# Kernel tuning notes

Measured on AMD Instinct MI355X. Metric: run time of the kernel, lower is better.

Reference implementation:

```python
import jax, jax.numpy as jnp
import numpy as np

HID = 768
NSPLITS = 12
HEAD_RATIO = 2
H = NSPLITS // HEAD_RATIO          # 6 attention heads
D = HID // NSPLITS                 # 64 head size
AH = H * D                         # 384 all_head_size
KS = 9                             # conv kernel size
PAD = (KS - 1) // 2
B, S = 4, 1024


def setup_inputs() -> dict:
    key = jax.random.key(0)
    ks = jax.random.split(key, 16)
    std = 0.02
    inp = {
        "Q": jax.random.normal(ks[0], (B, S, HID), jnp.float32),
        "K": jax.random.normal(ks[1], (B, S, HID), jnp.float32),
        "V": jax.random.normal(ks[2], (B, S, HID), jnp.float32),
        "td": jax.random.uniform(ks[3], (B, S), jnp.float32),
        "mask": jax.random.randint(ks[4], (B, S), 0, 2, jnp.int32),
        # projection weights, applied as x @ W (in, out)
        "Wq": jax.random.normal(ks[5], (HID, AH), jnp.float32) * std,
        "Wk": jax.random.normal(ks[6], (HID, AH), jnp.float32) * std,
        "Wv": jax.random.normal(ks[7], (HID, AH), jnp.float32) * std,
        # separable conv: depthwise (HID, KS), pointwise (AH, HID), bias (AH,)
        "dw_w": jax.random.normal(ks[8], (HID, KS), jnp.float32) * std,
        "pw_w": jax.random.normal(ks[9], (AH, HID), jnp.float32) * std,
        "sep_b": jnp.zeros((AH,), jnp.float32),
        # conv_kernel_layer Linear(AH -> H*KS)
        "ck_W": jax.random.normal(ks[10], (AH, H * KS), jnp.float32) * std,
        "ck_b": jnp.zeros((H * KS,), jnp.float32),
        # conv_out_layer Linear(HID -> AH)
        "co_W": jax.random.normal(ks[11], (HID, AH), jnp.float32) * std,
        "co_b": jnp.zeros((AH,), jnp.float32),
        # gammas init to zeros as in torch module
        "gammas": jnp.zeros((H, 1, 1), jnp.float32),
    }
    return inp


def dist_func(scores, td, am, gammas):
    # scores: [B,H,S,S]; am: [B,1,1,S] bool key mask; entirely non-differentiable.
    s = scores.shape[-1]
    dt = scores.dtype
    amf = am.astype(dt)
    p = jax.nn.softmax(jnp.where(am, scores, -1e8), axis=-1) * amf
    distcum = jnp.cumsum(p, axis=-1)
    disttotal = jnp.sum(p, axis=-1, keepdims=True)
    # |j - i| position distance
    pos = jnp.abs(jnp.arange(s)[None, :] - jnp.arange(s)[:, None]).astype(dt)
    dist_scores = jnp.sqrt(jnp.clip((disttotal - distcum) * pos[None, None], 0.0, None))
    gamma = -jax.nn.softplus(gammas)[None]  # (1,H,1,1)
    total_effect = jnp.clip(jnp.exp(dist_scores * gamma), 1e-5, 1e5)
    # time-distance effect on strictly-lower-triangular positions
    tdn = td / jnp.maximum(jnp.linalg.norm(td, axis=-1, keepdims=True), 1e-12)
    td_scores = jnp.broadcast_to(tdn[:, None, None, :], scores.shape)
    td_sm = jax.nn.softmax(jnp.where(am, td_scores, -1e4), axis=-1)
    lower = jnp.tril(jnp.ones((s, s), dt), -1)  # (triu == 0)
    return jax.lax.stop_gradient(total_effect - td_sm * lower[None, None])


def reference(Q, K, V, td, mask, Wq, Wk, Wv, dw_w, pw_w, sep_b, ck_W, ck_b, co_W, co_b, gammas):
    b, s, hid = Q.shape
    mq = Q @ Wq  # (B,S,AH)
    mk = K @ Wk
    mv = V @ Wv
    # SeparableConv1D over sequence dim of K
    x = jnp.transpose(K, (0, 2, 1))  # (B,HID,S)
    dw = jax.lax.conv_general_dilated(
        x, dw_w[:, None, :], window_strides=(1,), padding=[(PAD, PAD)],
        feature_group_count=hid, dimension_numbers=("NCH", "OIH", "NCH"))
    pw = jnp.einsum("bcs,oc->bos", dw, pw_w) + sep_b[None, :, None]
    mkc = jnp.transpose(pw, (0, 2, 1))  # (B,S,AH)

    q = mq.reshape(b, s, H, D).transpose(0, 2, 1, 3)
    k = mk.reshape(b, s, H, D).transpose(0, 2, 1, 3)
    v = mv.reshape(b, s, H, D).transpose(0, 2, 1, 3)

    # dynamic span convolution
    conv_attn = mkc * mq                                   # (B,S,AH)
    ck = (conv_attn @ ck_W + ck_b).reshape(b, s, H, KS)
    ck = jax.nn.softmax(ck, axis=-1)                       # per-position kernel
    co = V @ co_W + co_b                                   # (B,S,AH)
    co_pad = jnp.pad(co, ((0, 0), (PAD, PAD), (0, 0)))
    idx = jnp.arange(s)[:, None] + jnp.arange(KS)[None, :]  # (S,KS)
    unf = co_pad[:, idx, :].reshape(b, s, KS, H, D)         # sliding window gather
    conv_out = jnp.einsum("bskhd,bshk->bshd", unf, ck)      # (B,S,H,D)

    # attention with distance decay
    scores = jnp.einsum("bhid,bhjd->bhij", q, k) / np.float32(np.sqrt(D))
    am = (mask[:, None, None, :] != 0)  # (B,1,1,S) key mask
    total_effect = dist_func(scores, td, am, gammas)
    scores = jnp.where(am, scores * total_effect, -1e8)
    probs = jax.nn.softmax(scores, axis=-1)
    ctx = jnp.einsum("bhij,bhjd->bhid", probs, v).transpose(0, 2, 1, 3)  # (B,S,H,D)

    out = jnp.concatenate([ctx, conv_out], axis=2).reshape(b, s, HEAD_RATIO * AH)
    return out
```

## Files before the change

kernel.cpp:

```cpp
#include <hip/hip_runtime.h>
#include <hip/hip_bf16.h>

#define HIDC 768
#define Hh   6
#define Dd   64
#define AHc  384
#define KSc  9
#define PADc 4
#define Bb   4
#define Ss   1024
#define MRr  (Bb * Ss)

typedef __attribute__((ext_vector_type(8))) __bf16 bf16x8;
typedef __attribute__((ext_vector_type(4))) __bf16 bf16x4;
typedef __attribute__((ext_vector_type(4))) float  f32x4;

__device__ __forceinline__ void gl_lds16(const void* g, void* l) {
    __builtin_amdgcn_global_load_lds(
        (const __attribute__((address_space(1))) void*)g,
        (__attribute__((address_space(3))) void*)l, 16, 0, 0);
}

__device__ __forceinline__ void split8(const float* p, bf16x8& hi, bf16x8& lo) {
    float4 x0 = *(const float4*)p;
    float4 x1 = *(const float4*)(p + 4);
    float xs[8] = {x0.x, x0.y, x0.z, x0.w, x1.x, x1.y, x1.z, x1.w};
#pragma unroll
    for (int e = 0; e < 8; ++e) {
        __bf16 hv = (__bf16)xs[e];
        hi[e] = hv;
        lo[e] = (__bf16)(xs[e] - (float)hv);
    }
}

__device__ __forceinline__ void split8r(const float* xs, bf16x8& hi, bf16x8& lo) {
#pragma unroll
    for (int e = 0; e < 8; ++e) {
        __bf16 hv = (__bf16)xs[e];
        hi[e] = hv;
        lo[e] = (__bf16)(xs[e] - (float)hv);
    }
}

__device__ __forceinline__ bf16x8 cvt8(const float* p) {
    float4 x0 = *(const float4*)p;
    float4 x1 = *(const float4*)(p + 4);
    float xs[8] = {x0.x, x0.y, x0.z, x0.w, x1.x, x1.y, x1.z, x1.w};
    bf16x8 h;
#pragma unroll
    for (int e = 0; e < 8; ++e) h[e] = (__bf16)xs[e];
    return h;
}

__global__ void k_depthwise(const float* __restrict__ Kin, const float* __restrict__ dww,
                            __bf16* __restrict__ dwbf) {
    int idx = blockIdx.x * 256 + threadIdx.x;
    if (idx >= Bb * Ss * HIDC / 4) return;
    int c4 = idx % (HIDC / 4);
    int s  = (idx / (HIDC / 4)) % Ss;
    int b  = idx / ((HIDC / 4) * Ss);
    int c  = c4 * 4;
    float wv[4][KSc];
#pragma unroll
    for (int j = 0; j < 4; ++j)
#pragma unroll
        for (int k = 0; k < KSc; ++k) wv[j][k] = dww[(c + j) * KSc + k];
    float4 acc = {0.f, 0.f, 0.f, 0.f};
#pragma unroll
    for (int k = 0; k < KSc; ++k) {
        int sp = s + k - PADc;
        if (sp >= 0 && sp < Ss) {
            float4 v = *(const float4*)&Kin[(size_t)(b * Ss + sp) * HIDC + c];
            acc.x += v.x * wv[0][k]; acc.y += v.y * wv[1][k];
            acc.z += v.z * wv[2][k]; acc.w += v.w * wv[3][k];
        }
    }
    bf16x4 o = {(__bf16)acc.x, (__bf16)acc.y, (__bf16)acc.z, (__bf16)acc.w};
    *(bf16x4*)(dwbf + (size_t)idx * 4) = o;
}

__global__ __launch_bounds__(256) void k_wsplit_t(const float* __restrict__ Wq, const float* __restrict__ Wk,
                                                  const float* __restrict__ Wv, const float* __restrict__ coW,
                                                  __bf16* __restrict__ Whi, __bf16* __restrict__ Wlo) {
    int z = blockIdx.z;
    const float* src = (z == 0) ? Wq : (z == 1) ? Wk : (z == 2) ? Wv : coW;
    int n0 = blockIdx.x * 64, k0 = blockIdx.y * 64;
    int tid = threadIdx.x;
    int r = tid >> 2, cq = tid & 3;
    __shared__ float tile[64][65];
#pragma unroll
    for (int e = 0; e < 4; ++e) {
        float4 v = *(const float4*)&src[(size_t)(k0 + r) * AHc + n0 + cq * 16 + e * 4];
        tile[r][cq * 16 + e * 4 + 0] = v.x;
        tile[r][cq * 16 + e * 4 + 1] = v.y;
        tile[r][cq * 16 + e * 4 + 2] = v.z;
        tile[r][cq * 16 + e * 4 + 3] = v.w;
    }
    __syncthreads();
    float x[16];
#pragma unroll
    for (int e = 0; e < 16; ++e) x[e] = tile[cq * 16 + e][r];
    bf16x8 h0, l0, h1, l1;
    split8r(x, h0, l0);
    split8r(x + 8, h1, l1);
    size_t dst = ((size_t)(z * AHc + n0 + r)) * HIDC + k0 + cq * 16;
    *(bf16x8*)(Whi + dst)     = h0;
    *(bf16x8*)(Whi + dst + 8) = h1;
    *(bf16x8*)(Wlo + dst)     = l0;
    *(bf16x8*)(Wlo + dst + 8) = l1;
}

__global__ void k_wsplit_c(const float* __restrict__ pww,
                           __bf16* __restrict__ Whi, __bf16* __restrict__ Wlo) {
    int idx = blockIdx.x * 256 + threadIdx.x;
    if (idx >= AHc * HIDC / 8) return;
    bf16x8 hi, lo;
    split8(pww + (size_t)idx * 8, hi, lo);
    size_t dst = (size_t)4 * AHc * HIDC + (size_t)idx * 8;
    *(bf16x8*)(Whi + dst) = hi;
    *(bf16x8*)(Wlo + dst) = lo;
}

__global__ void k_absplit(const float* __restrict__ Q, const float* __restrict__ V,
                          __bf16* __restrict__ qbf, __bf16* __restrict__ vbf) {
    const int n8 = MRr * HIDC / 8;
    int idx = blockIdx.x * 256 + threadIdx.x;
    if (idx >= 2 * n8) return;
    if (idx < n8) {
        *(bf16x8*)(qbf + (size_t)idx * 8) = cvt8(Q + (size_t)idx * 8);
    } else {
        int i = idx - n8;
        *(bf16x8*)(vbf + (size_t)i * 8) = cvt8(V + (size_t)i * 8);
    }
}

__global__ void k_qkvsplit(const float* __restrict__ mq, __bf16* __restrict__ qh) {
    int idx = blockIdx.x * 256 + threadIdx.x;
    if (idx >= MRr * AHc / 8) return;
    *(bf16x8*)(qh + (size_t)idx * 8) = cvt8(mq + (size_t)idx * 8);
}

__global__ __launch_bounds__(256) void k_vtrans(const float* __restrict__ mv,
                                                __bf16* __restrict__ vt) {
    int s0 = blockIdx.x * 64;
    int h = blockIdx.y % Hh, b = blockIdx.y / Hh;
    int tid = threadIdx.x;
    int r = tid >> 2, cq = tid & 3;
    __shared__ float tile[64][65];
    const float* src = mv + (size_t)(b * Ss + s0 + r) * AHc + h * Dd + cq * 16;
#pragma unroll
    for (int e = 0; e < 4; ++e) {
        float4 v = *(const float4*)(src + e * 4);
        tile[r][cq * 16 + e * 4 + 0] = v.x;
        tile[r][cq * 16 + e * 4 + 1] = v.y;
        tile[r][cq * 16 + e * 4 + 2] = v.z;
        tile[r][cq * 16 + e * 4 + 3] = v.w;
    }
    __syncthreads();
    bf16x8 o0, o1;
#pragma unroll
    for (int e = 0; e < 8; ++e) {
        o0[e] = (__bf16)tile[cq * 16 + e][r];
        o1[e] = (__bf16)tile[cq * 16 + 8 + e][r];
    }
    __bf16* dst = vt + ((size_t)((b * Hh + h) * Dd + r)) * Ss + s0 + cq * 16;
    *(bf16x8*)dst       = o0;
    *(bf16x8*)(dst + 8) = o1;
}

__global__ void k_bias(const float* __restrict__ cob, const float* __restrict__ sepb,
                       float* __restrict__ biasb) {
    int idx = blockIdx.x * 256 + threadIdx.x;
    if (idx >= 5 * AHc) return;
    int z = idx / AHc, n = idx % AHc;
    biasb[idx] = (z == 3) ? cob[n] : (z == 4) ? sepb[n] : 0.f;
}

__global__ __launch_bounds__(256) void k_gemm5(
        const __bf16* __restrict__ qbf, const float* __restrict__ Kin,
        const __bf16* __restrict__ vbf, const __bf16* __restrict__ dwbf,
        const __bf16* __restrict__ Whi, const __bf16* __restrict__ Wlo,
        const float* __restrict__ biasb, float* __restrict__ Call,
        __bf16* __restrict__ kh, __bf16* __restrict__ kl) {
    __shared__ __attribute__((aligned(16))) __bf16 As [128 * 32];
    __shared__ __attribute__((aligned(16))) __bf16 BsH[128 * 32];
    __shared__ __attribute__((aligned(16))) __bf16 BsL[128 * 32];

    int wg = blockIdx.x + 3 * (blockIdx.y + 32 * blockIdx.z);
    int n2 = (wg & 7) * 60 + (wg >> 3);
    int bxx = n2 % 3, byy = (n2 / 3) % 32, z = n2 / 96;

    int m0 = byy * 128, n0 = bxx * 128;
    int tid = threadIdx.x;
    int wave = tid >> 6, lane = tid & 63, quad = lane >> 4, l15 = lane & 15;

    int lrow = lane >> 2;
    int lswz = 8 * ((lane & 3) ^ (lrow & 3));

    int brow = wave * 32 + lrow;
    const __bf16* BhG0 = Whi + ((size_t)(z * AHc + n0 + brow)) * HIDC + lswz;
    const __bf16* BhG1 = BhG0 + (size_t)16 * HIDC;
    const __bf16* BlG0 = Wlo + ((size_t)(z * AHc + n0 + brow)) * HIDC + lswz;
    const __bf16* BlG1 = BlG0 + (size_t)16 * HIDC;
    __bf16* BhL0 = BsH + (wave * 2 + 0) * 512;
    __bf16* BhL1 = BsH + (wave * 2 + 1) * 512;
    __bf16* BlL0 = BsL + (wave * 2 + 0) * 512;
    __bf16* BlL1 = BsL + (wave * 2 + 1) * 512;

    const __bf16* Abf = (z == 0) ? qbf : (z == 4) ? dwbf : vbf;
    const __bf16* AG0 = Abf + ((size_t)(m0 + wave * 32 + lrow)) * HIDC + lswz;
    const __bf16* AG1 = AG0 + (size_t)16 * HIDC;
    __bf16* AL0 = As + (wave * 2 + 0) * 512;
    __bf16* AL1 = As + (wave * 2 + 1) * 512;

    int sr = tid >> 1;
    int sk = (tid & 1) * 16;
    const float* Arow = Kin + (size_t)(m0 + sr) * HIDC + sk;
    int g0 = sk >> 3;
    int d0 = sr * 32 + ((g0       ^ (sr & 3)) * 8);
    int d1 = sr * 32 + (((g0 + 1) ^ (sr & 3)) * 8);

    int swz = (quad ^ (l15 & 3)) * 8;
    f32x4 acc[4][4] = {};

    for (int k0 = 0; k0 < HIDC; k0 += 32) {
        if (z == 1) {
            const float* ap = Arow + k0;
            *(bf16x8*)&As[d0] = cvt8(ap);
            *(bf16x8*)&As[d1] = cvt8(ap + 8);
        } else {
            gl_lds16(AG0 + k0, AL0);
            gl_lds16(AG1 + k0, AL1);
        }
        gl_lds16(BhG0 + k0, BhL0);
        gl_lds16(BhG1 + k0, BhL1);
        gl_lds16(BlG0 + k0, BlL0);
        gl_lds16(BlG1 + k0, BlL1);
        __syncthreads();

        int mrow = (wave >> 1) * 64 + l15;
        int nrow = (wave & 1) * 64 + l15;
        bf16x8 ah[4], bh[4], bl[4];
#pragma unroll
        for (int mt = 0; mt < 4; ++mt)
            ah[mt] = *(bf16x8*)&As[(mrow + mt * 16) * 32 + swz];
#pragma unroll
        for (int nt = 0; nt < 4; ++nt) {
            bh[nt] = *(bf16x8*)&BsH[(nrow + nt * 16) * 32 + swz];
            bl[nt] = *(bf16x8*)&BsL[(nrow + nt * 16) * 32 + swz];
        }
#pragma unroll
        for (int mt = 0; mt < 4; ++mt)
#pragma unroll
            for (int nt = 0; nt < 4; ++nt) {
                acc[mt][nt] = __builtin_amdgcn_mfma_f32_16x16x32_bf16(ah[mt], bh[nt], acc[mt][nt], 0, 0, 0);
                acc[mt][nt] = __builtin_amdgcn_mfma_f32_16x16x32_bf16(ah[mt], bl[nt], acc[mt][nt], 0, 0, 0);
            }
        __syncthreads();
    }

    if (z == 1) {
#pragma unroll
        for (int nt = 0; nt < 4; ++nt) {
            int n = n0 + (wave & 1) * 64 + nt * 16 + l15;
#pragma unroll
            for (int mt = 0; mt < 4; ++mt) {
#pragma unroll
                for (int r = 0; r < 4; ++r) {
                    int m = m0 + (wave >> 1) * 64 + mt * 16 + quad * 4 + r;
                    float v = acc[mt][nt][r];
                    __bf16 hv = (__bf16)v;
                    kh[(size_t)m * AHc + n] = hv;
                    kl[(size_t)m * AHc + n] = (__bf16)(v - (float)hv);
                }
            }
        }
    } else {
        float* Cz = Call + (size_t)z * MRr * AHc;
        const float* bz = biasb + z * AHc;
#pragma unroll
        for (int nt = 0; nt < 4; ++nt) {
            int n = n0 + (wave & 1) * 64 + nt * 16 + l15;
            float bias = bz[n];
#pragma unroll
            for (int mt = 0; mt < 4; ++mt) {
#pragma unroll
                for (int r = 0; r < 4; ++r) {
                    int m = m0 + (wave >> 1) * 64 + mt * 16 + quad * 4 + r;
                    Cz[(size_t)m * AHc + n] = acc[mt][nt][r] + bias;
                }
            }
        }
    }
}

__global__ __launch_bounds__(64) void k_ck(const float* __restrict__ mkc, const float* __restrict__ mq,
                                           const float* __restrict__ ckW, const float* __restrict__ ckb,
                                           float* __restrict__ ck_sm) {
    int row = blockIdx.x;
    int tid = threadIdx.x;
    __shared__ float ca[AHc];
    __shared__ float ckv[Hh * KSc];
    for (int o = tid; o < AHc; o += 64)
        ca[o] = mkc[row * AHc + o] * mq[row * AHc + o];
    __syncthreads();
    if (tid < Hh * KSc) {
        float acc = ckb[tid];
        for (int o = 0; o < AHc; ++o)
            acc += ca[o] * ckW[o * (Hh * KSc) + tid];
        ckv[tid] = acc;
    }
    __syncthreads();
    if (tid < Hh) {
        float m = -3e38f;
#pragma unroll
        for (int k = 0; k < KSc; ++k) m = fmaxf(m, ckv[tid * KSc + k]);
        float e[KSc];
        float s = 0.f;
#pragma unroll
        for (int k = 0; k < KSc; ++k) { e[k] = expf(ckv[tid * KSc + k] - m); s += e[k]; }
        float inv = 1.f / s;
#pragma unroll
        for (int k = 0; k < KSc; ++k) ck_sm[(row * Hh + tid) * KSc + k] = e[k] * inv;
    }
}

__global__ void k_convout(const float* __restrict__ co, const float* __restrict__ ck_sm,
                          float* __restrict__ out) {
    int idx = blockIdx.x * 256 + threadIdx.x;
    if (idx >= Bb * Ss * AHc / 4) return;
    int d4 = idx & 15;
    int h  = (idx >> 4) % Hh;
    int s  = (idx / (AHc / 4)) % Ss;
    int b  = idx / ((AHc / 4) * Ss);
    int row = b * Ss + s;
    const float* ck = ck_sm + (size_t)(row * Hh + h) * KSc;
    float4 acc = {0.f, 0.f, 0.f, 0.f};
#pragma unroll
    for (int k = 0; k < KSc; ++k) {
        int sp = s + k - PADc;
        if (sp >= 0 && sp < Ss) {
            float4 v = *(const float4*)&co[(size_t)(b * Ss + sp) * AHc + h * Dd + d4 * 4];
            float wv = ck[k];
            acc.x += wv * v.x; acc.y += wv * v.y; acc.z += wv * v.z; acc.w += wv * v.w;
        }
    }
    *(float4*)&out[(size_t)row * (2 * AHc) + AHc + h * Dd + d4 * 4] = acc;
}

__global__ __launch_bounds__(256) void k_td(const float* __restrict__ td, const int* __restrict__ mask,
                                            float* __restrict__ td_sm) {
    int b = blockIdx.x;
    int tid = threadIdx.x;
    __shared__ float red[256];
    __shared__ float tv[Ss];
    float ls = 0.f;
    for (int j = tid; j < Ss; j += 256) {
        float v = td[b * Ss + j];
        tv[j] = v;
        ls += v * v;
    }
    red[tid] = ls; __syncthreads();
    for (int s = 128; s > 0; s >>= 1) { if (tid < s) red[tid] += red[tid + s]; __syncthreads(); }
    float norm = fmaxf(sqrtf(red[0]), 1e-12f);
    __syncthreads();
    float lm = -3e38f;
    for (int j = tid; j < Ss; j += 256) {
        float v = mask[b * Ss + j] ? tv[j] / norm : -1e4f;
        tv[j] = v;
        lm = fmaxf(lm, v);
    }
    red[tid] = lm; __syncthreads();
    for (int s = 128; s > 0; s >>= 1) { if (tid < s) red[tid] = fmaxf(red[tid], red[tid + s]); __syncthreads(); }
    float m = red[0]; __syncthreads();
    float lsum = 0.f;
    for (int j = tid; j < Ss; j += 256) {
        float e = expf(tv[j] - m);
        tv[j] = e;
        lsum += e;
    }
    red[tid] = lsum; __syncthreads();
    for (int s = 128; s > 0; s >>= 1) { if (tid < s) red[tid] += red[tid + s]; __syncthreads(); }
    float inv = 1.f / red[0];
    __syncthreads();
    for (int j = tid; j < Ss; j += 256)
        td_sm[b * Ss + j] = tv[j] * inv;
}

__device__ __forceinline__ int scix(int m, int j) {
    return m * 1024 + (j ^ (((m ^ (j >> 6)) & 7) << 2));
}

__global__ __launch_bounds__(512) void k_attn(const __bf16* __restrict__ qh,
                                              const __bf16* __restrict__ kh, const __bf16* __restrict__ kl,
                                              const __bf16* __restrict__ vt,
                                              const int* __restrict__ mask,
                                              const float* __restrict__ td_sm, const float* __restrict__ gammas,
                                              float* __restrict__ out) {
    __shared__ float sc[16 * 1024];
    int wg = blockIdx.x + 64 * blockIdx.y;
    int n  = (wg & 7) * 192 + (wg >> 3);
    int bx = n & 63, by = n >> 6;
    int i0 = bx * 16;
    int h = by % Hh, b = by / Hh;
    int tid = threadIdx.x;
    int w = tid >> 6, lane = tid & 63, quad = lane >> 4, l15 = lane & 15;
    int jw = w * 128;

    bf16x8 a_hi[2];
    {
        size_t qoff = (size_t)(b * Ss + i0 + l15) * AHc + h * Dd + quad * 8;
        a_hi[0] = *(const bf16x8*)(qh + qoff);
        a_hi[1] = *(const bf16x8*)(qh + qoff + 32);
    }
#pragma unroll 2
    for (int t = 0; t < 8; ++t) {
        int jt = jw + t * 16;
        size_t koff = (size_t)(b * Ss + jt + l15) * AHc + h * Dd + quad * 8;
        f32x4 acc = {0.f, 0.f, 0.f, 0.f};
#pragma unroll
        for (int kc = 0; kc < 2; ++kc) {
            bf16x8 khv = *(const bf16x8*)(kh + koff + kc * 32);
            bf16x8 klv = *(const bf16x8*)(kl + koff + kc * 32);
            acc = __builtin_amdgcn_mfma_f32_16x16x32_bf16(a_hi[kc], khv, acc, 0, 0, 0);
            acc = __builtin_amdgcn_mfma_f32_16x16x32_bf16(a_hi[kc], klv, acc, 0, 0, 0);
        }
#pragma unroll
        for (int r = 0; r < 4; ++r)
            sc[scix(quad * 4 + r, jt + l15)] = acc[r] * 0.125f;
    }
    __syncthreads();

    const int* mrow = mask + b * Ss;
    const float* tdrow = td_sm + b * Ss;
    float gamma = -log1pf(expf(gammas[h]));
    int jb = lane << 4;
    __attribute__((aligned(16))) int marr[16];
    {
        const int4* mp = (const int4*)(mrow + jb);
#pragma unroll
        for (int k = 0; k < 4; ++k) ((int4*)marr)[k] = mp[k];
    }
    __attribute__((aligned(16))) float tdv[16];
    {
        const float4* tp = (const float4*)(tdrow + jb);
#pragma unroll
        for (int k = 0; k < 4; ++k) ((float4*)tdv)[k] = tp[k];
    }

#pragma unroll
    for (int r4 = 0; r4 < 2; ++r4) {
        int m = w * 2 + r4;
        int i = i0 + m;
        __attribute__((aligned(16))) float s[16];
        float p[16];
#pragma unroll
        for (int g = 0; g < 4; ++g)
            *(f32x4*)(s + 4 * g) = *(const f32x4*)&sc[scix(m, jb + 4 * g)];
        float mx = -1e30f;
#pragma unroll
        for (int jj = 0; jj < 16; ++jj) mx = fmaxf(mx, marr[jj] ? s[jj] : -1e30f);
        mx = fmaxf(mx, __shfl_xor(mx, 1));  mx = fmaxf(mx, __shfl_xor(mx, 2));
        mx = fmaxf(mx, __shfl_xor(mx, 4));  mx = fmaxf(mx, __shfl_xor(mx, 8));
        mx = fmaxf(mx, __shfl_xor(mx, 16)); mx = fmaxf(mx, __shfl_xor(mx, 32));
#pragma unroll
        for (int jj = 0; jj < 16; ++jj) p[jj] = marr[jj] ? __expf(s[jj] - mx) : 0.f;
#pragma unroll
        for (int jj = 1; jj < 16; ++jj) p[jj] += p[jj - 1];
        float t = p[15];
        float incl = t;
#pragma unroll
        for (int dlt = 1; dlt < 64; dlt <<= 1) {
            float v = __shfl_up(incl, dlt);
            if (lane >= dlt) incl += v;
        }
        float off = incl - t;
        float tot = __shfl(incl, 63);
        float inv = 1.f / fmaxf(tot, 1e-30f);
        float mx2 = -1e30f;
#pragma unroll
        for (int jj = 0; jj < 16; ++jj) {
            int j = jb + jj;
            float cum = p[jj] + off;
            float pos = fabsf((float)(j - i));
            float ds = sqrtf(fmaxf((tot - cum) * inv * pos, 0.f));
            float te = fminf(fmaxf(__expf(ds * gamma), 1e-5f), 1e5f);
            float mult = te - ((j < i) ? tdv[jj] : 0.f);
            float s2 = marr[jj] ? s[jj] * mult : -1e8f;
            s[jj] = s2;
            mx2 = fmaxf(mx2, s2);
        }
        mx2 = fmaxf(mx2, __shfl_xor(mx2, 1));  mx2 = fmaxf(mx2, __shfl_xor(mx2, 2));
        mx2 = fmaxf(mx2, __shfl_xor(mx2, 4));  mx2 = fmaxf(mx2, __shfl_xor(mx2, 8));
        mx2 = fmaxf(mx2, __shfl_xor(mx2, 16)); mx2 = fmaxf(mx2, __shfl_xor(mx2, 32));
        float sm = 0.f;
#pragma unroll
        for (int jj = 0; jj < 16; ++jj) { s[jj] = __expf(s[jj] - mx2); sm += s[jj]; }
        sm += __shfl_xor(sm, 1);  sm += __shfl_xor(sm, 2);
        sm += __shfl_xor(sm, 4);  sm += __shfl_xor(sm, 8);
        sm += __shfl_xor(sm, 16); sm += __shfl_xor(sm, 32);
        float inv2 = 1.f / sm;
#pragma unroll
        for (int jj = 0; jj < 16; ++jj) s[jj] *= inv2;
#pragma unroll
        for (int g = 0; g < 4; ++g)
            *(f32x4*)&sc[scix(m, jb + 4 * g)] = *(const f32x4*)(s + 4 * g);
    }
    __syncthreads();

    f32x4 oacc[4] = {};
    const __bf16* vtb = vt + (size_t)(b * Hh + h) * Dd * Ss;
#pragma unroll
    for (int kc = 0; kc < 4; ++kc) {
        int j0 = jw + kc * 32 + quad * 8;
        __attribute__((aligned(16))) float x[8];
        *(f32x4*)x       = *(const f32x4*)&sc[scix(l15, j0)];
        *(f32x4*)(x + 4) = *(const f32x4*)&sc[scix(l15, j0 + 4)];
        bf16x8 p_hi, p_lo;
        split8r(x, p_hi, p_lo);
#pragma unroll
        for (int nt = 0; nt < 4; ++nt) {
            int d = nt * 16 + l15;
            bf16x8 vv = *(const bf16x8*)(vtb + (size_t)d * Ss + j0);
            oacc[nt] = __builtin_amdgcn_mfma_f32_16x16x32_bf16(p_hi, vv, oacc[nt], 0, 0, 0);
            oacc[nt] = __builtin_amdgcn_mfma_f32_16x16x32_bf16(p_lo, vv, oacc[nt], 0, 0, 0);
        }
    }
    __syncthreads();
#pragma unroll
    for (int nt = 0; nt < 4; ++nt)
#pragma unroll
        for (int r = 0; r < 4; ++r)
            sc[w * 1024 + (quad * 4 + r) * 64 + nt * 16 + l15] = oacc[nt][r];
    __syncthreads();
#pragma unroll
    for (int e = 0; e < 2; ++e) {
        int idx = e * 512 + tid;
        int m = idx >> 6, dd = idx & 63;
        float v = 0.f;
#pragma unroll
        for (int ww = 0; ww < 8; ++ww) v += sc[ww * 1024 + idx];
        out[(size_t)(b * Ss + i0 + m) * (2 * AHc) + h * Dd + dd] = v;
    }
}

extern "C" void kernel_launch(void* const* d_in, const int* in_sizes, int n_in,
                              void* d_out, int out_size, void* d_ws, size_t ws_size,
                              hipStream_t stream) {
    const float* Q    = (const float*)d_in[0];
    const float* Kin  = (const float*)d_in[1];
    const float* V    = (const float*)d_in[2];
    const float* td   = (const float*)d_in[3];
    const int*   mask = (const int*)d_in[4];
    const float* Wq   = (const float*)d_in[5];
    const float* Wk   = (const float*)d_in[6];
    const float* Wv   = (const float*)d_in[7];
    const float* dww  = (const float*)d_in[8];
    const float* pww  = (const float*)d_in[9];
    const float* sepb = (const float*)d_in[10];
    const float* ckW  = (const float*)d_in[11];
    const float* ckb  = (const float*)d_in[12];
    const float* coW  = (const float*)d_in[13];
    const float* cob  = (const float*)d_in[14];
    const float* gam  = (const float*)d_in[15];
    float* out = (float*)d_out;
    float* ws = (float*)d_ws;

    float* mq    = ws;
    float* mks   = mq    + (size_t)MRr * AHc;
    float* mv    = mks   + (size_t)MRr * AHc;
    float* co    = mv    + (size_t)MRr * AHc;
    float* mkc   = co    + (size_t)MRr * AHc;
    float* dwr   = mkc   + (size_t)MRr * AHc;
    float* cksm  = dwr   + (size_t)MRr * HIDC;
    float* tdsm  = cksm  + (size_t)MRr * Hh * KSc;
    float* biasb = tdsm  + (size_t)Bb * Ss;

    __bf16* dwbf = (__bf16*)dwr;
    __bf16* qbf  = (__bf16*)(dwr + (size_t)MRr * HIDC / 2);
    __bf16* qh   = (__bf16*)dwr;
    __bf16* vt   = (__bf16*)(dwr + (size_t)MRr * HIDC / 2);
    __bf16* kh = (__bf16*)mks;
    __bf16* kl = kh + (size_t)MRr * AHc;

    __bf16* Whi = (__bf16*)d_out;
    __bf16* Wlo = Whi + (size_t)5 * AHc * HIDC;
    __bf16* vbf = Wlo + (size_t)5 * AHc * HIDC;

    dim3 gt(AHc / 64, HIDC / 64, 4);
    k_wsplit_t<<<gt, 256, 0, stream>>>(Wq, Wk, Wv, coW, Whi, Wlo);
    k_wsplit_c<<<(AHc * HIDC / 8 + 255) / 256, 256, 0, stream>>>(pww, Whi, Wlo);
    k_absplit<<<(2 * MRr * HIDC / 8 + 255) / 256, 256, 0, stream>>>(Q, V, qbf, vbf);
    k_depthwise<<<(MRr * HIDC / 4 + 255) / 256, 256, 0, stream>>>(Kin, dww, dwbf);
    k_bias<<<(5 * AHc + 255) / 256, 256, 0, stream>>>(cob, sepb, biasb);

    dim3 gg(AHc / 128, MRr / 128, 5);
    k_gemm5<<<gg, 256, 0, stream>>>(qbf, Kin, vbf, dwbf, Whi, Wlo, biasb, mq, kh, kl);

    k_qkvsplit<<<(MRr * AHc / 8 + 255) / 256, 256, 0, stream>>>(mq, qh);
    k_vtrans<<<dim3(Ss / 64, Bb * Hh), 256, 0, stream>>>(mv, vt);
    k_ck<<<MRr, 64, 0, stream>>>(mkc, mq, ckW, ckb, cksm);
    k_convout<<<(MRr * AHc / 4 + 255) / 256, 256, 0, stream>>>(co, cksm, out);
    k_td<<<Bb, 256, 0, stream>>>(td, mask, tdsm);

    dim3 ga(Ss / 16, Bb * Hh);
    k_attn<<<ga, 512, 0, stream>>>(qh, kh, kl, vt, mask, tdsm, gam, out);
}
```

Baseline: 303.4 us.

## Fold small prep kernels together and emit bf16 Q/V-transposed from GEMM epilogue

Merges the depthwise conv with the Q/V bf16 casts into one launch, and merges the pointwise-weight split, bias setup and td softmax into one misc kernel. The GEMM epilogue now writes bf16 Q directly (alongside fp32 mq needed by the conv path) and writes V already transposed as bf16. This removes the separate qkvsplit and vtrans kernels and their fp32 re-reads. Workspace layout changes so vt/qh live in the former mv region. The scattered transposed stores of V from the epilogue may be less coalesced than the tiled transpose.

Result: faster. 281.7 us (-7.2%).

```diff
diff --git a/kernel.cpp b/kernel.cpp
--- a/kernel.cpp
+++ b/kernel.cpp
@@ -52,31 +52,44 @@
     return h;
 }
 
-__global__ void k_depthwise(const float* __restrict__ Kin, const float* __restrict__ dww,
-                            __bf16* __restrict__ dwbf) {
-    int idx = blockIdx.x * 256 + threadIdx.x;
-    if (idx >= Bb * Ss * HIDC / 4) return;
-    int c4 = idx % (HIDC / 4);
-    int s  = (idx / (HIDC / 4)) % Ss;
-    int b  = idx / ((HIDC / 4) * Ss);
-    int c  = c4 * 4;
-    float wv[4][KSc];
-#pragma unroll
-    for (int j = 0; j < 4; ++j)
-#pragma unroll
-        for (int k = 0; k < KSc; ++k) wv[j][k] = dww[(c + j) * KSc + k];
-    float4 acc = {0.f, 0.f, 0.f, 0.f};
-#pragma unroll
-    for (int k = 0; k < KSc; ++k) {
-        int sp = s + k - PADc;
-        if (sp >= 0 && sp < Ss) {
-            float4 v = *(const float4*)&Kin[(size_t)(b * Ss + sp) * HIDC + c];
-            acc.x += v.x * wv[0][k]; acc.y += v.y * wv[1][k];
-            acc.z += v.z * wv[2][k]; acc.w += v.w * wv[3][k];
-        }
-    }
-    bf16x4 o = {(__bf16)acc.x, (__bf16)acc.y, (__bf16)acc.z, (__bf16)acc.w};
-    *(bf16x4*)(dwbf + (size_t)idx * 4) = o;
+__global__ void k_dwab(const float* __restrict__ Kin, const float* __restrict__ dww,
+                       const float* __restrict__ Q, const float* __restrict__ V,
+                       __bf16* __restrict__ dwbf,
+                       __bf16* __restrict__ qbf, __bf16* __restrict__ vbf) {
+    int bid = blockIdx.x;
+    if (bid < 3072) {
+        int idx = bid * 256 + threadIdx.x;
+        int c4 = idx % (HIDC / 4);
+        int s  = (idx / (HIDC / 4)) % Ss;
+        int b  = idx / ((HIDC / 4) * Ss);
+        int c  = c4 * 4;
+        float wv[4][KSc];
+#pragma unroll
+        for (int j = 0; j < 4; ++j)
+#pragma unroll
+            for (int k = 0; k < KSc; ++k) wv[j][k] = dww[(c + j) * KSc + k];
+        float4 acc = {0.f, 0.f, 0.f, 0.f};
+#pragma unroll
+        for (int k = 0; k < KSc; ++k) {
+            int sp = s + k - PADc;
+            if (sp >= 0 && sp < Ss) {
+                float4 v = *(const float4*)&Kin[(size_t)(b * Ss + sp) * HIDC + c];
+                acc.x += v.x * wv[0][k]; acc.y += v.y * wv[1][k];
+                acc.z += v.z * wv[2][k]; acc.w += v.w * wv[3][k];
+            }
+        }
+        bf16x4 o = {(__bf16)acc.x, (__bf16)acc.y, (__bf16)acc.z, (__bf16)acc.w};
+        *(bf16x4*)(dwbf + (size_t)idx * 4) = o;
+    } else {
+        const int n8 = MRr * HIDC / 8;
+        int idx = (bid - 3072) * 256 + threadIdx.x;
+        if (idx < n8) {
+            *(bf16x8*)(qbf + (size_t)idx * 8) = cvt8(Q + (size_t)idx * 8);
+        } else {
+            int i = idx - n8;
+            *(bf16x8*)(vbf + (size_t)i * 8) = cvt8(V + (size_t)i * 8);
+        }
+    }
 }
 
 __global__ __launch_bounds__(256) void k_wsplit_t(const float* __restrict__ Wq, const float* __restrict__ Wk,
@@ -110,70 +123,64 @@
     *(bf16x8*)(Wlo + dst + 8) = l1;
 }
 
-__global__ void k_wsplit_c(const float* __restrict__ pww,
-                           __bf16* __restrict__ Whi, __bf16* __restrict__ Wlo) {
-    int idx = blockIdx.x * 256 + threadIdx.x;
-    if (idx >= AHc * HIDC / 8) return;
-    bf16x8 hi, lo;
-    split8(pww + (size_t)idx * 8, hi, lo);
-    size_t dst = (size_t)4 * AHc * HIDC + (size_t)idx * 8;
-    *(bf16x8*)(Whi + dst) = hi;
-    *(bf16x8*)(Wlo + dst) = lo;
-}
-
-__global__ void k_absplit(const float* __restrict__ Q, const float* __restrict__ V,
-                          __bf16* __restrict__ qbf, __bf16* __restrict__ vbf) {
-    const int n8 = MRr * HIDC / 8;
-    int idx = blockIdx.x * 256 + threadIdx.x;
-    if (idx >= 2 * n8) return;
-    if (idx < n8) {
-        *(bf16x8*)(qbf + (size_t)idx * 8) = cvt8(Q + (size_t)idx * 8);
-    } else {
-        int i = idx - n8;
-        *(bf16x8*)(vbf + (size_t)i * 8) = cvt8(V + (size_t)i * 8);
-    }
-}
-
-__global__ void k_qkvsplit(const float* __restrict__ mq, __bf16* __restrict__ qh) {
-    int idx = blockIdx.x * 256 + threadIdx.x;
-    if (idx >= MRr * AHc / 8) return;
-    *(bf16x8*)(qh + (size_t)idx * 8) = cvt8(mq + (size_t)idx * 8);
-}
-
-__global__ __launch_bounds__(256) void k_vtrans(const float* __restrict__ mv,
-                                                __bf16* __restrict__ vt) {
-    int s0 = blockIdx.x * 64;
-    int h = blockIdx.y % Hh, b = blockIdx.y / Hh;
+__global__ __launch_bounds__(256) void k_misc(const float* __restrict__ pww,
+                                              const float* __restrict__ cob, const float* __restrict__ sepb,
+                                              const float* __restrict__ td, const int* __restrict__ mask,
+                                              __bf16* __restrict__ Whi, __bf16* __restrict__ Wlo,
+                                              float* __restrict__ biasb, float* __restrict__ td_sm) {
+    int bid = blockIdx.x;
     int tid = threadIdx.x;
-    int r = tid >> 2, cq = tid & 3;
-    __shared__ float tile[64][65];
-    const float* src = mv + (size_t)(b * Ss + s0 + r) * AHc + h * Dd + cq * 16;
-#pragma unroll
-    for (int e = 0; e < 4; ++e) {
-        float4 v = *(const float4*)(src + e * 4);
-        tile[r][cq * 16 + e * 4 + 0] = v.x;
-        tile[r][cq * 16 + e * 4 + 1] = v.y;
-        tile[r][cq * 16 + e * 4 + 2] = v.z;
-        tile[r][cq * 16 + e * 4 + 3] = v.w;
-    }
-    __syncthreads();
-    bf16x8 o0, o1;
-#pragma unroll
-    for (int e = 0; e < 8; ++e) {
-        o0[e] = (__bf16)tile[cq * 16 + e][r];
-        o1[e] = (__bf16)tile[cq * 16 + 8 + e][r];
-    }
-    __bf16* dst = vt + ((size_t)((b * Hh + h) * Dd + r)) * Ss + s0 + cq * 16;
-    *(bf16x8*)dst       = o0;
-    *(bf16x8*)(dst + 8) = o1;
-}
-
-__global__ void k_bias(const float* __restrict__ cob, const float* __restrict__ sepb,
-                       float* __restrict__ biasb) {
-    int idx = blockIdx.x * 256 + threadIdx.x;
-    if (idx >= 5 * AHc) return;
-    int z = idx / AHc, n = idx % AHc;
-    biasb[idx] = (z == 3) ? cob[n] : (z == 4) ? sepb[n] : 0.f;
+    if (bid < 144) {
+        int idx = bid * 256 + tid;
+        bf16x8 hi, lo;
+        split8(pww + (size_t)idx * 8, hi, lo);
+        size_t dst = (size_t)4 * AHc * HIDC + (size_t)idx * 8;
+        *(bf16x8*)(Whi + dst) = hi;
+        *(bf16x8*)(Wlo + dst) = lo;
+        return;
+    }
+    if (bid < 152) {
+        int idx = (bid - 144) * 256 + tid;
+        if (idx < 5 * AHc) {
+            int z = idx / AHc, n = idx % AHc;
+            biasb[idx] = (z == 3) ? cob[n] : (z == 4) ? sepb[n] : 0.f;
+        }
+        return;
+    }
+    int b = bid - 152;
+    __shared__ float red[256];
+    __shared__ float tv[Ss];
+    float ls = 0.f;
+    for (int j = tid; j < Ss; j += 256) {
+        float v = td[b * Ss + j];
+        tv[j] = v;
+        ls += v * v;
+    }
+    red[tid] = ls; __syncthreads();
+    for (int s = 128; s > 0; s >>= 1) { if (tid < s) red[tid] += red[tid + s]; __syncthreads(); }
+    float norm = fmaxf(sqrtf(red[0]), 1e-12f);
+    __syncthreads();
+    float lm = -3e38f;
+    for (int j = tid; j < Ss; j += 256) {
+        float v = mask[b * Ss + j] ? tv[j] / norm : -1e4f;
+        tv[j] = v;
+        lm = fmaxf(lm, v);
+    }
+    red[tid] = lm; __syncthreads();
+    for (int s = 128; s > 0; s >>= 1) { if (tid < s) red[tid] = fmaxf(red[tid], red[tid + s]); __syncthreads(); }
+    float m = red[0]; __syncthreads();
+    float lsum = 0.f;
+    for (int j = tid; j < Ss; j += 256) {
+        float e = expf(tv[j] - m);
+        tv[j] = e;
+        lsum += e;
+    }
+    red[tid] = lsum; __syncthreads();
+    for (int s = 128; s > 0; s >>= 1) { if (tid < s) red[tid] += red[tid + s]; __syncthreads(); }
+    float inv = 1.f / red[0];
+    __syncthreads();
+    for (int j = tid; j < Ss; j += 256)
+        td_sm[b * Ss + j] = tv[j] * inv;
 }
 
 __global__ __launch_bounds__(256) void k_gemm5(
@@ -181,7 +188,8 @@
         const __bf16* __restrict__ vbf, const __bf16* __restrict__ dwbf,
         const __bf16* __restrict__ Whi, const __bf16* __restrict__ Wlo,
         const float* __restrict__ biasb, float* __restrict__ Call,
-        __bf16* __restrict__ kh, __bf16* __restrict__ kl) {
+        __bf16* __restrict__ kh, __bf16* __restrict__ kl,
+        __bf16* __restrict__ qh, __bf16* __restrict__ vt) {
     __shared__ __attribute__((aligned(16))) __bf16 As [128 * 32];
     __shared__ __attribute__((aligned(16))) __bf16 BsH[128 * 32];
     __shared__ __attribute__((aligned(16))) __bf16 BsL[128 * 32];
@@ -272,6 +280,37 @@
                     __bf16 hv = (__bf16)v;
                     kh[(size_t)m * AHc + n] = hv;
                     kl[(size_t)m * AHc + n] = (__bf16)(v - (float)hv);
+                }
+            }
+        }
+    } else if (z == 2) {
+        int b = m0 >> 10;
+#pragma unroll
+        for (int nt = 0; nt < 4; ++nt) {
+            int n = (wave & 1) * 64 + nt * 16 + l15;
+            int gn = n0 + n;
+            int h = gn >> 6, d = gn & 63;
+#pragma unroll
+            for (int mt = 0; mt < 4; ++mt) {
+                int m = m0 + (wave >> 1) * 64 + mt * 16 + quad * 4;
+                int s = m & (Ss - 1);
+                bf16x4 o = {(__bf16)acc[mt][nt][0], (__bf16)acc[mt][nt][1],
+                            (__bf16)acc[mt][nt][2], (__bf16)acc[mt][nt][3]};
+                *(bf16x4*)&vt[((size_t)((b * Hh + h) * Dd + d)) * Ss + s] = o;
+            }
+        }
+    } else if (z == 0) {
+#pragma unroll
+        for (int nt = 0; nt < 4; ++nt) {
+            int n = n0 + (wave & 1) * 64 + nt * 16 + l15;
+#pragma unroll
+            for (int mt = 0; mt < 4; ++mt) {
+#pragma unroll
+                for (int r = 0; r < 4; ++r) {
+                    int m = m0 + (wave >> 1) * 64 + mt * 16 + quad * 4 + r;
+                    float v = acc[mt][nt][r];
+                    Call[(size_t)m * AHc + n] = v;
+                    qh[(size_t)m * AHc + n] = (__bf16)v;
                 }
             }
         }
@@ -346,45 +385,6 @@
         }
     }
     *(float4*)&out[(size_t)row * (2 * AHc) + AHc + h * Dd + d4 * 4] = acc;
-}
-
-__global__ __launch_bounds__(256) void k_td(const float* __restrict__ td, const int* __restrict__ mask,
-                                            float* __restrict__ td_sm) {
-    int b = blockIdx.x;
-    int tid = threadIdx.x;
-    __shared__ float red[256];
-    __shared__ float tv[Ss];
-    float ls = 0.f;
-    for (int j = tid; j < Ss; j += 256) {
-        float v = td[b * Ss + j];
-        tv[j] = v;
-        ls += v * v;
-    }
-    red[tid] = ls; __syncthreads();
-    for (int s = 128; s > 0; s >>= 1) { if (tid < s) red[tid] += red[tid + s]; __syncthreads(); }
-    float norm = fmaxf(sqrtf(red[0]), 1e-12f);
-    __syncthreads();
-    float lm = -3e38f;
-    for (int j = tid; j < Ss; j += 256) {
-        float v = mask[b * Ss + j] ? tv[j] / norm : -1e4f;
-        tv[j] = v;
-        lm = fmaxf(lm, v);
-    }
-    red[tid] = lm; __syncthreads();
-    for (int s = 128; s > 0; s >>= 1) { if (tid < s) red[tid] = fmaxf(red[tid], red[tid + s]); __syncthreads(); }
-    float m = red[0]; __syncthreads();
-    float lsum = 0.f;
-    for (int j = tid; j < Ss; j += 256) {
-        float e = expf(tv[j] - m);
-        tv[j] = e;
-        lsum += e;
-    }
-    red[tid] = lsum; __syncthreads();
-    for (int s = 128; s > 0; s >>= 1) { if (tid < s) red[tid] += red[tid + s]; __syncthreads(); }
-    float inv = 1.f / red[0];
-    __syncthreads();
-    for (int j = tid; j < Ss; j += 256)
-        td_sm[b * Ss + j] = tv[j] * inv;
 }
 
 __device__ __forceinline__ int scix(int m, int j) {
@@ -568,8 +568,8 @@
 
     float* mq    = ws;
     float* mks   = mq    + (size_t)MRr * AHc;
-    float* mv    = mks   + (size_t)MRr * AHc;
-    float* co    = mv    + (size_t)MRr * AHc;
+    float* mvs   = mks   + (size_t)MRr * AHc;
+    float* co    = mvs   + (size_t)MRr * AHc;
     float* mkc   = co    + (size_t)MRr * AHc;
     float* dwr   = mkc   + (size_t)MRr * AHc;
     float* cksm  = dwr   + (size_t)MRr * HIDC;
@@ -578,10 +578,10 @@
 
     __bf16* dwbf = (__bf16*)dwr;
     __bf16* qbf  = (__bf16*)(dwr + (size_t)MRr * HIDC / 2);
-    __bf16* qh   = (__bf16*)dwr;
-    __bf16* vt   = (__bf16*)(dwr + (size_t)MRr * HIDC / 2);
     __bf16* kh = (__bf16*)mks;
     __bf16* kl = kh + (size_t)MRr * AHc;
+    __bf16* vt = (__bf16*)mvs;
+    __bf16* qh = vt + (size_t)MRr * AHc;
 
     __bf16* Whi = (__bf16*)d_out;
     __bf16* Wlo = Whi + (size_t)5 * AHc * HIDC;
@@ -589,19 +589,14 @@
 
     dim3 gt(AHc / 64, HIDC / 64, 4);
     k_wsplit_t<<<gt, 256, 0, stream>>>(Wq, Wk, Wv, coW, Whi, Wlo);
-    k_wsplit_c<<<(AHc * HIDC / 8 + 255) / 256, 256, 0, stream>>>(pww, Whi, Wlo);
-    k_absplit<<<(2 * MRr * HIDC / 8 + 255) / 256, 256, 0, stream>>>(Q, V, qbf, vbf);
-    k_depthwise<<<(MRr * HIDC / 4 + 255) / 256, 256, 0, stream>>>(Kin, dww, dwbf);
-    k_bias<<<(5 * AHc + 255) / 256, 256, 0, stream>>>(cob, sepb, biasb);
+    k_misc<<<156, 256, 0, stream>>>(pww, cob, sepb, td, mask, Whi, Wlo, biasb, tdsm);
+    k_dwab<<<6144, 256, 0, stream>>>(Kin, dww, Q, V, dwbf, qbf, vbf);
 
     dim3 gg(AHc / 128, MRr / 128, 5);
-    k_gemm5<<<gg, 256, 0, stream>>>(qbf, Kin, vbf, dwbf, Whi, Wlo, biasb, mq, kh, kl);
-
-    k_qkvsplit<<<(MRr * AHc / 8 + 255) / 256, 256, 0, stream>>>(mq, qh);
-    k_vtrans<<<dim3(Ss / 64, Bb * Hh), 256, 0, stream>>>(mv, vt);
+    k_gemm5<<<gg, 256, 0, stream>>>(qbf, Kin, vbf, dwbf, Whi, Wlo, biasb, mq, kh, kl, qh, vt);
+
     k_ck<<<MRr, 64, 0, stream>>>(mkc, mq, ckW, ckb, cksm);
     k_convout<<<(MRr * AHc / 4 + 255) / 256, 256, 0, stream>>>(co, cksm, out);
-    k_td<<<Bb, 256, 0, stream>>>(td, mask, tdsm);
 
     dim3 ga(Ss / 16, Bb * Hh);
     k_attn<<<ga, 512, 0, stream>>>(qh, kh, kl, vt, mask, tdsm, gam, out);
```
